# Optimization experiments

Hardware: AMD Instinct MI355X
Metric: run time of the kernel (lower is better)

Reference implementation:

```python
import jax, jax.numpy as jnp
import numpy as np

B, N, D, S = 4, 8, 64, 8192  # batch, heads, dim_head, seq_len


def setup_inputs() -> dict:
    key = jax.random.key(0)
    kq, kk, kv = jax.random.split(key, 3)
    q = jax.random.normal(kq, (B, N, D, S), dtype=jnp.float32)
    k = jax.random.normal(kk, (B, N, D, S), dtype=jnp.float32)
    v = jax.random.normal(kv, (B, N, D, S), dtype=jnp.float32)
    return {"q": q, "k": k, "v": v}


def reference(q, k, v):
    # q, k, v: [b, n, d, s] = [batch, heads, dim_head, seq]
    scale = q.shape[-2] ** -0.5  # dim_head^-0.5
    qs = jax.nn.softmax(q, axis=-2) * scale   # softmax over feature dim
    ks = jax.nn.softmax(k, axis=-1)           # softmax over seq dim
    # kv context: [b, n, d, d] -- avoids the O(s^2) score matrix
    context = jnp.einsum('bnis,bnjs->bnij', ks, v)
    # out: [b, n, d, s]
    return jnp.einsum('bnij,bnis->bnjs', context, qs)
```

## Files before the change

### kernel.cpp

```cpp
#include <hip/hip_runtime.h>
#include <math.h>


typedef _Float16 half8 __attribute__((ext_vector_type(8)));
typedef float floatx4 __attribute__((ext_vector_type(4)));
typedef float floatx16 __attribute__((ext_vector_type(16)));

constexpr int BHEADS = 32;
constexpr int DH     = 64;
constexpr int SEQ    = 8192;
constexpr int NCHUNK = 32;
constexpr float QSCALE = 0.125f;

__global__ __launch_bounds__(256)
void ctx_partial_kernel(const float* __restrict__ K, const float* __restrict__ V,
                        float* __restrict__ partial, float* __restrict__ Zp)
{
    const int head  = blockIdx.y;
    const int chunk = blockIdx.x;
    const int t     = threadIdx.x;
    const int lane  = t & 63;
    const int w     = t >> 6;
    const int ln    = lane & 15;
    const int q8    = lane >> 4;

    const int s0 = chunk * 256;
    const float* ka = K + (size_t)head * DH * SEQ
                        + (size_t)(16 * w + ln) * SEQ + s0 + q8 * 8;
    const float* va = V + (size_t)head * DH * SEQ
                        + (size_t)ln * SEQ + s0 + q8 * 8;

    floatx4 acc[4];
    #pragma unroll
    for (int jt = 0; jt < 4; ++jt) acc[jt] = (floatx4){0.f, 0.f, 0.f, 0.f};
    float zacc = 0.f;

    float4 cak[2][2];
    float4 cbv[2][4][2];

    cak[0][0] = *(const float4*)(ka);
    cak[0][1] = *(const float4*)(ka + 4);
    #pragma unroll
    for (int jt = 0; jt < 4; ++jt) {
        cbv[0][jt][0] = *(const float4*)(va + (size_t)jt * 16 * SEQ);
        cbv[0][jt][1] = *(const float4*)(va + (size_t)jt * 16 * SEQ + 4);
    }

    #pragma unroll
    for (int kk = 0; kk < 8; ++kk) {
        const int cur = kk & 1;
        const int nxt = cur ^ 1;
        if (kk < 7) {
            const int off = (kk + 1) * 32;
            cak[nxt][0] = *(const float4*)(ka + off);
            cak[nxt][1] = *(const float4*)(ka + off + 4);
            #pragma unroll
            for (int jt = 0; jt < 4; ++jt) {
                cbv[nxt][jt][0] = *(const float4*)(va + (size_t)jt * 16 * SEQ + off);
                cbv[nxt][jt][1] = *(const float4*)(va + (size_t)jt * 16 * SEQ + off + 4);
            }
        }
        float e[8];
        e[0] = __expf(cak[cur][0].x); e[1] = __expf(cak[cur][0].y);
        e[2] = __expf(cak[cur][0].z); e[3] = __expf(cak[cur][0].w);
        e[4] = __expf(cak[cur][1].x); e[5] = __expf(cak[cur][1].y);
        e[6] = __expf(cak[cur][1].z); e[7] = __expf(cak[cur][1].w);
        zacc += e[0]+e[1]+e[2]+e[3]+e[4]+e[5]+e[6]+e[7];
        half8 ah;
        #pragma unroll
        for (int x = 0; x < 8; ++x) ah[x] = (_Float16)e[x];
        #pragma unroll
        for (int jt = 0; jt < 4; ++jt) {
            half8 bh;
            bh[0] = (_Float16)cbv[cur][jt][0].x; bh[1] = (_Float16)cbv[cur][jt][0].y;
            bh[2] = (_Float16)cbv[cur][jt][0].z; bh[3] = (_Float16)cbv[cur][jt][0].w;
            bh[4] = (_Float16)cbv[cur][jt][1].x; bh[5] = (_Float16)cbv[cur][jt][1].y;
            bh[6] = (_Float16)cbv[cur][jt][1].z; bh[7] = (_Float16)cbv[cur][jt][1].w;
            acc[jt] = __builtin_amdgcn_mfma_f32_16x16x32_f16(ah, bh, acc[jt], 0, 0, 0);
        }
    }

    float* ph = partial + (size_t)(head * NCHUNK + chunk) * DH * DH;
    #pragma unroll
    for (int jt = 0; jt < 4; ++jt) {
        #pragma unroll
        for (int rr = 0; rr < 4; ++rr) {
            const int i = 16 * w + q8 * 4 + rr;
            const int j = 16 * jt + ln;
            ph[i * DH + j] = acc[jt][rr];
        }
    }

    zacc += __shfl_xor(zacc, 16);
    zacc += __shfl_xor(zacc, 32);
    if (lane < 16)
        Zp[(head * NCHUNK + chunk) * DH + 16 * w + ln] = zacc;
}

__global__ __launch_bounds__(256)
void reduce_kernel(const float* __restrict__ partial, const float* __restrict__ Zp,
                   _Float16* __restrict__ czT)
{
    const int h  = blockIdx.x >> 4;
    const int ig = blockIdx.x & 15;
    const int t  = threadIdx.x;
    const int il = t >> 6;
    const int j  = t & 63;
    const int i  = 4 * ig + il;

    const float* ph = partial + (size_t)h * NCHUNK * DH * DH + i * DH + j;
    float sum = 0.f;
    #pragma unroll
    for (int c = 0; c < NCHUNK; ++c)
        sum += ph[(size_t)c * DH * DH];

    float z = 0.f;
    #pragma unroll
    for (int c = 0; c < NCHUNK; ++c)
        z += Zp[(h * NCHUNK + c) * DH + i];

    czT[(size_t)h * DH * DH + j * DH + i] = (_Float16)(sum / z);
}

__global__ __launch_bounds__(256)
void out_kernel(const float* __restrict__ Q, const _Float16* __restrict__ czT,
                float* __restrict__ out)
{
    const int head = blockIdx.y;
    const int sb   = blockIdx.x;
    const int t    = threadIdx.x;
    const int lane = t & 63;
    const int w    = t >> 6;
    const int l31  = lane & 31;
    const int lh   = lane >> 5;
    const int jw   = 32 * (w & 1);
    const int sw   = 32 * (w >> 1);

    __shared__ __align__(16) float    qf[64 * 68];
    __shared__ __align__(16) _Float16 eqT[64 * 64];
    __shared__ __align__(16) float    wred[64 * 4];

    const float* qh = Q + (size_t)head * DH * SEQ;
    const int r0 = t >> 4;
    const int sc = 4 * (t & 15);
    const int s0 = sb * 128;

    float4 pq[4];
    #pragma unroll
    for (int p = 0; p < 4; ++p)
        pq[p] = *(const float4*)(qh + (size_t)(r0 + 16 * p) * SEQ + s0 + sc);

    const _Float16* ch = czT + (size_t)head * DH * DH;
    half8 afr[4];
    #pragma unroll
    for (int st = 0; st < 4; ++st)
        afr[st] = *(const half8*)(ch + (jw + l31) * DH + st * 16 + lh * 8);

    for (int r = 0; r < 2; ++r) {
        #pragma unroll
        for (int p = 0; p < 4; ++p)
            *(float4*)(qf + (r0 + 16 * p) * 68 + sc) = pq[p];
        if (r < 1) {
            #pragma unroll
            for (int p = 0; p < 4; ++p)
                pq[p] = *(const float4*)(qh + (size_t)(r0 + 16 * p) * SEQ
                                         + s0 + 64 + sc);
        }
        __syncthreads();
        {
            const int s  = t & 63;
            const int cg = t >> 6;
            float wsum = 0.f;
            #pragma unroll
            for (int h2 = 0; h2 < 2; ++h2) {
                const int cc = cg + 4 * h2;
                half8 p8;
                #pragma unroll
                for (int jj = 0; jj < 8; ++jj) {
                    const float e = __expf(qf[(8 * cc + jj) * 68 + s]);
                    wsum += e;
                    p8[jj] = (_Float16)e;
                }
                *(half8*)(eqT + s * 64 + ((cc ^ (s & 7)) * 8)) = p8;
            }
            wred[s * 4 + cg] = wsum;
        }
        __syncthreads();
        const float4 wv = *(const float4*)(wred + (sw + l31) * 4);
        const float rw = QSCALE / (wv.x + wv.y + wv.z + wv.w);
        floatx16 acc = {};
        #pragma unroll
        for (int st = 0; st < 4; ++st) {
            const int s2 = sw + l31;
            const int cc = 2 * st + lh;
            const half8 b = *(const half8*)(eqT + s2 * 64 + ((cc ^ (s2 & 7)) * 8));
            acc = __builtin_amdgcn_mfma_f32_32x32x16_f16(afr[st], b, acc, 0, 0, 0);
        }
        float* oh = out + (size_t)head * DH * SEQ + s0 + r * 64;
        #pragma unroll
        for (int rg = 0; rg < 16; ++rg) {
            const int j = jw + (rg & 3) + 8 * (rg >> 2) + 4 * lh;
            oh[(size_t)j * SEQ + sw + l31] = acc[rg] * rw;
        }
    }
}

extern "C" void kernel_launch(void* const* d_in, const int* in_sizes, int n_in,
                              void* d_out, int out_size, void* d_ws, size_t ws_size,
                              hipStream_t stream)
{
    const float* q = (const float*)d_in[0];
    const float* k = (const float*)d_in[1];
    const float* v = (const float*)d_in[2];
    float* out = (float*)d_out;

    float*    partial = (float*)d_ws;
    float*    Zp      = partial + BHEADS * NCHUNK * DH * DH;
    _Float16* czT     = (_Float16*)(Zp + BHEADS * NCHUNK * DH);

    ctx_partial_kernel<<<dim3(NCHUNK, BHEADS), 256, 0, stream>>>(k, v, partial, Zp);
    reduce_kernel<<<BHEADS * 16, 256, 0, stream>>>(partial, Zp, czT);
    out_kernel<<<dim3(64, BHEADS), 256, 0, stream>>>(q, czT, out);
}
```

Baseline: 241.4 us.

## Stage K and V tiles through double-buffered swizzled LDS in ctx kernel

The context-partial kernel now loads each 64x32 K and V tile into shared memory once per block, using row-contiguous 128-byte segments per row. It double-buffers those tiles with a register prefetch of the next step, and XOR-swizzles the LDS slots to avoid bank conflicts. Before, every wave read the same V rows straight from global memory as strided 32-byte pieces. The change targets that redundant, poorly coalesced global traffic, at the cost of a block barrier each step and extra LDS reads and writes.

Result: slower. 247.0 us (+2.3%).

```diff
diff --git a/kernel.cpp b/kernel.cpp
--- a/kernel.cpp
+++ b/kernel.cpp
@@ -25,58 +25,87 @@
     const int q8    = lane >> 4;
 
     const int s0 = chunk * 256;
-    const float* ka = K + (size_t)head * DH * SEQ
-                        + (size_t)(16 * w + ln) * SEQ + s0 + q8 * 8;
-    const float* va = V + (size_t)head * DH * SEQ
-                        + (size_t)ln * SEQ + s0 + q8 * 8;
+    const float* kh = K + (size_t)head * DH * SEQ;
+    const float* vh = V + (size_t)head * DH * SEQ;
+
+    __shared__ __align__(16) float kbuf[2][64 * 32];
+    __shared__ __align__(16) float vbuf[2][64 * 32];
+
+    const int srow  = t >> 3;
+    const int sslot = t & 7;
+    const int wslot = sslot ^ (srow & 7);
+
+    float4 stK[2], stV[2];
+    #pragma unroll
+    for (int q = 0; q < 2; ++q) {
+        const int r = q * 32 + srow;
+        stK[q] = *(const float4*)(kh + (size_t)r * SEQ + s0 + sslot * 4);
+        stV[q] = *(const float4*)(vh + (size_t)r * SEQ + s0 + sslot * 4);
+    }
+    #pragma unroll
+    for (int q = 0; q < 2; ++q) {
+        const int r = q * 32 + srow;
+        *(float4*)(&kbuf[0][r * 32 + wslot * 4]) = stK[q];
+        *(float4*)(&vbuf[0][r * 32 + wslot * 4]) = stV[q];
+    }
+    __syncthreads();
 
     floatx4 acc[4];
     #pragma unroll
     for (int jt = 0; jt < 4; ++jt) acc[jt] = (floatx4){0.f, 0.f, 0.f, 0.f};
     float zacc = 0.f;
 
-    float4 cak[2][2];
-    float4 cbv[2][4][2];
-
-    cak[0][0] = *(const float4*)(ka);
-    cak[0][1] = *(const float4*)(ka + 4);
-    #pragma unroll
-    for (int jt = 0; jt < 4; ++jt) {
-        cbv[0][jt][0] = *(const float4*)(va + (size_t)jt * 16 * SEQ);
-        cbv[0][jt][1] = *(const float4*)(va + (size_t)jt * 16 * SEQ + 4);
-    }
-
-    #pragma unroll
-    for (int kk = 0; kk < 8; ++kk) {
-        const int cur = kk & 1;
-        const int nxt = cur ^ 1;
-        if (kk < 7) {
-            const int off = (kk + 1) * 32;
-            cak[nxt][0] = *(const float4*)(ka + off);
-            cak[nxt][1] = *(const float4*)(ka + off + 4);
-            #pragma unroll
-            for (int jt = 0; jt < 4; ++jt) {
-                cbv[nxt][jt][0] = *(const float4*)(va + (size_t)jt * 16 * SEQ + off);
-                cbv[nxt][jt][1] = *(const float4*)(va + (size_t)jt * 16 * SEQ + off + 4);
+    const int rA = 16 * w + ln;
+
+    #pragma unroll 2
+    for (int step = 0; step < 8; ++step) {
+        const int p = step & 1;
+        if (step < 7) {
+            const int sb = s0 + (step + 1) * 32;
+            #pragma unroll
+            for (int q = 0; q < 2; ++q) {
+                const int r = q * 32 + srow;
+                stK[q] = *(const float4*)(kh + (size_t)r * SEQ + sb + sslot * 4);
+                stV[q] = *(const float4*)(vh + (size_t)r * SEQ + sb + sslot * 4);
             }
         }
         float e[8];
-        e[0] = __expf(cak[cur][0].x); e[1] = __expf(cak[cur][0].y);
-        e[2] = __expf(cak[cur][0].z); e[3] = __expf(cak[cur][0].w);
-        e[4] = __expf(cak[cur][1].x); e[5] = __expf(cak[cur][1].y);
-        e[6] = __expf(cak[cur][1].z); e[7] = __expf(cak[cur][1].w);
+        #pragma unroll
+        for (int eo = 0; eo < 2; ++eo) {
+            const int sl = ((q8 * 2 + eo) ^ (rA & 7)) * 4;
+            const float4 kv = *(const float4*)(&kbuf[p][rA * 32 + sl]);
+            e[eo * 4 + 0] = __expf(kv.x);
+            e[eo * 4 + 1] = __expf(kv.y);
+            e[eo * 4 + 2] = __expf(kv.z);
+            e[eo * 4 + 3] = __expf(kv.w);
+        }
         zacc += e[0]+e[1]+e[2]+e[3]+e[4]+e[5]+e[6]+e[7];
         half8 ah;
         #pragma unroll
         for (int x = 0; x < 8; ++x) ah[x] = (_Float16)e[x];
         #pragma unroll
         for (int jt = 0; jt < 4; ++jt) {
+            const int rB = 16 * jt + ln;
             half8 bh;
-            bh[0] = (_Float16)cbv[cur][jt][0].x; bh[1] = (_Float16)cbv[cur][jt][0].y;
-            bh[2] = (_Float16)cbv[cur][jt][0].z; bh[3] = (_Float16)cbv[cur][jt][0].w;
-            bh[4] = (_Float16)cbv[cur][jt][1].x; bh[5] = (_Float16)cbv[cur][jt][1].y;
-            bh[6] = (_Float16)cbv[cur][jt][1].z; bh[7] = (_Float16)cbv[cur][jt][1].w;
+            #pragma unroll
+            for (int eo = 0; eo < 2; ++eo) {
+                const int sl = ((q8 * 2 + eo) ^ (rB & 7)) * 4;
+                const float4 vv = *(const float4*)(&vbuf[p][rB * 32 + sl]);
+                bh[eo * 4 + 0] = (_Float16)vv.x;
+                bh[eo * 4 + 1] = (_Float16)vv.y;
+                bh[eo * 4 + 2] = (_Float16)vv.z;
+                bh[eo * 4 + 3] = (_Float16)vv.w;
+            }
             acc[jt] = __builtin_amdgcn_mfma_f32_16x16x32_f16(ah, bh, acc[jt], 0, 0, 0);
+        }
+        if (step < 7) {
+            #pragma unroll
+            for (int q = 0; q < 2; ++q) {
+                const int r = q * 32 + srow;
+                *(float4*)(&kbuf[p ^ 1][r * 32 + wslot * 4]) = stK[q];
+                *(float4*)(&vbuf[p ^ 1][r * 32 + wslot * 4]) = stV[q];
+            }
+            __syncthreads();
         }
     }
 
```
